# Optimization experiments

Measured on AMD Instinct MI355X. Metric: run time of the kernel, lower is better.

The kernel has to match this reference:

```python
import jax, jax.numpy as jnp
import numpy as np
from jax import lax

K_NEI = 64      # max_num_neighbors in radius query
NEG = -1e30     # mask value for max-aggregation


def fps(pos, n_sample):
    """Farthest point sampling per cloud. pos: [B,N,3] -> idx [B,n_sample] int32.
    Deterministic start at point 0 (PyG uses a random start)."""
    B, N, _ = pos.shape
    start = jnp.zeros((B,), jnp.int32)
    big = jnp.full((B, N), jnp.finfo(pos.dtype).max, pos.dtype)
    def body(carry, _):
        mind, last = carry
        lp = jnp.take_along_axis(pos, last[:, None, None], axis=1)  # [B,1,3]
        d = jnp.sum((pos - lp) ** 2, -1)                            # [B,N]
        mind = jnp.minimum(mind, d)
        nxt = jnp.argmax(mind, axis=1).astype(jnp.int32)
        return (mind, nxt), nxt
    (_, _), rest = lax.scan(body, (big, start), None, length=n_sample - 1)
    return jnp.concatenate([start[None], rest], 0).T  # [B, n_sample]


def radius_nn(pos_all, pos_q, r, k):
    """Up to k nearest neighbors within radius r (per cloud).
    pos_all: [B,N,3], pos_q: [B,M,3] -> idx [B,M,k] int32, valid [B,M,k] bool."""
    d2 = jnp.sum((pos_q[:, :, None, :] - pos_all[:, None, :, :]) ** 2, -1)  # [B,M,N]
    score = jnp.where(d2 <= r * r, -d2, -jnp.inf)
    vals, idx = lax.top_k(score, k)
    return idx, jnp.isfinite(vals)


def gather(feat, idx):
    """feat: [B,P,C], idx: [B,M,k] -> [B,M,k,C]"""
    B, M, k = idx.shape
    out = jnp.take_along_axis(feat, idx.reshape(B, M * k)[:, :, None], axis=1)
    return out.reshape(B, M, k, feat.shape[-1])


def mlp3(x, w1, b1, w2, b2, w3, b3):
    x = jax.nn.relu(x @ w1 + b1)
    x = jax.nn.relu(x @ w2 + b2)
    return x @ w3 + b3


def point_conv(x, pos_src, pos_dst, nidx, valid, params):
    """PyG PointConv: message = local_nn([x_j, pos_j - pos_i]), max aggregation."""
    rel = gather(pos_src, nidx) - pos_dst[:, :, None, :]          # [B,M,k,3]
    msg = rel if x is None else jnp.concatenate([gather(x, nidx), rel], -1)
    h = mlp3(msg, *params)                                        # [B,M,k,C]
    h = jnp.where(valid[..., None], h, NEG)
    out = jnp.max(h, axis=2)
    return jnp.where(valid.any(2)[..., None], out, 0.0)


def setup_inputs() -> dict:
    key = jax.random.key(0)
    shapes = {
        'sa1_w1': (3, 64), 'sa1_b1': (64,), 'sa1_w2': (64, 64), 'sa1_b2': (64,),
        'sa1_w3': (64, 128), 'sa1_b3': (128,),
        'sa2_w1': (131, 128), 'sa2_b1': (128,), 'sa2_w2': (128, 128), 'sa2_b2': (128,),
        'sa2_w3': (128, 256), 'sa2_b3': (256,),
        'g_w1': (259, 256), 'g_b1': (256,), 'g_w2': (256, 512), 'g_b2': (512,),
        'g_w3': (512, 1024), 'g_b3': (1024,),
        'l1_w': (1024, 512), 'l1_b': (512,), 'l2_w': (512, 256), 'l2_b': (256,),
        'l3_w': (256, 7), 'l3_b': (7,),
    }
    ks = jax.random.split(key, len(shapes) + 1)
    inp = {'points': jax.random.uniform(ks[0], (8, 4096, 3), jnp.float32)}
    for i, (name, shp) in enumerate(shapes.items()):
        inp[name] = jax.random.normal(ks[i + 1], shp, jnp.float32) / np.sqrt(shp[0]).astype(np.float32)
    return inp


def reference(points, sa1_w1, sa1_b1, sa1_w2, sa1_b2, sa1_w3, sa1_b3,
              sa2_w1, sa2_b1, sa2_w2, sa2_b2, sa2_w3, sa2_b3,
              g_w1, g_b1, g_w2, g_b2, g_w3, g_b3,
              l1_w, l1_b, l2_w, l2_b, l3_w, l3_b):
    B, N, _ = points.shape
    pos = points[..., :3]
    # ---- stage 1: fps ratio 0.5, radius 0.1 ----
    N1 = N // 2
    idx1 = fps(pos, N1)
    pos1 = jnp.take_along_axis(pos, idx1[..., None], axis=1)      # [B,N1,3]
    nidx1, valid1 = radius_nn(pos, pos1, 0.1, K_NEI)
    x1 = jax.nn.relu(point_conv(None, pos, pos1, nidx1, valid1,
                                (sa1_w1, sa1_b1, sa1_w2, sa1_b2, sa1_w3, sa1_b3)))
    # ---- stage 2: fps ratio 0.25, radius 0.2 ----
    N2 = N1 // 4
    idx2 = fps(pos1, N2)
    pos2 = jnp.take_along_axis(pos1, idx2[..., None], axis=1)     # [B,N2,3]
    nidx2, valid2 = radius_nn(pos1, pos2, 0.2, K_NEI)
    x2 = jax.nn.relu(point_conv(x1, pos1, pos2, nidx2, valid2,
                                (sa2_w1, sa2_b1, sa2_w2, sa2_b2, sa2_w3, sa2_b3)))
    # ---- global MLP + grouped maxpool over 128 points ----
    g = mlp3(jnp.concatenate([x2, pos2], -1), g_w1, g_b1, g_w2, g_b2, g_w3, g_b3)  # [B,N2,1024]
    g = g.reshape(-1, 128, 1024).max(axis=1)                      # [B*N2/128, 1024]
    h = jax.nn.relu(g @ l1_w + l1_b)                              # dropout = identity (eval)
    h = jax.nn.relu(h @ l2_w + l2_b)
    h = h @ l3_w + l3_b                                           # [B*N2/128, 7]
    b_out = h.reshape(B, -1, 7).mean(axis=1)                      # [B,7]
    t = b_out[:, :3]
    q = b_out[:, 3:]
    q = q / jnp.maximum(jnp.linalg.norm(q, axis=-1, keepdims=True), 1e-12)
    return jnp.concatenate([t, q], axis=-1)
```

## Files before the change

### kernel.cpp

```cpp
#include <hip/hip_runtime.h>
#include <float.h>


typedef float f32x2 __attribute__((ext_vector_type(2)));

__device__ __forceinline__ float d2_rn(float ax, float ay, float az,
                                       float bx, float by, float bz) {
  float dx = __fsub_rn(ax, bx), dy = __fsub_rn(ay, by), dz = __fsub_rn(az, bz);
  return __fadd_rn(__fadd_rn(__fmul_rn(dx, dx), __fmul_rn(dy, dy)), __fmul_rn(dz, dz));
}

template<int CTRL>
__device__ __forceinline__ unsigned long long dppmax(unsigned long long a) {
  const unsigned int lo = (unsigned int)a, hi = (unsigned int)(a >> 32);
  const unsigned int slo =
      (unsigned int)__builtin_amdgcn_update_dpp(0, (int)lo, CTRL, 0xf, 0xf, true);
  const unsigned int shi =
      (unsigned int)__builtin_amdgcn_update_dpp(0, (int)hi, CTRL, 0xf, 0xf, true);
  const unsigned long long s = ((unsigned long long)shi << 32) | slo;
  return s > a ? s : a;
}

template<int N, int NS, int T>
__global__ __launch_bounds__(T) void fps_kernel(const float* __restrict__ pos,
                                                float* __restrict__ posq) {
  constexpr int P = N / T;
  constexpr int W = T / 64;
  __shared__ float4 s_xyz[N];
  __shared__ unsigned long long s_red[2][W];
  const int t = threadIdx.x, b = blockIdx.x;
  const float* pb = pos + (size_t)b * N * 3;
  for (int i = t; i < N; i += T)
    s_xyz[i] = make_float4(pb[i*3+0], pb[i*3+1], pb[i*3+2], 0.f);
  __syncthreads();
  float px[P], py[P], pz[P], mind[P];
  unsigned int kc[P];
#pragma unroll
  for (int j = 0; j < P; ++j) {
    const float4 c = s_xyz[j*T + t];
    px[j] = c.x; py[j] = c.y; pz[j] = c.z;
    mind[j] = FLT_MAX;
    kc[j] = (unsigned int)(N - 1 - (j*T + t));
  }
  float lx = s_xyz[0].x, ly = s_xyz[0].y, lz = s_xyz[0].z;
  float* outp = posq + (size_t)b * NS * 3;
  if (t == 0) { outp[0] = lx; outp[1] = ly; outp[2] = lz; }
  for (int it = 1; it < NS; ++it) {
    float bv = -1.0f; unsigned int bk = 0;
#pragma unroll
    for (int j = 0; j < P; ++j) {
      const float dx = __fsub_rn(px[j], lx);
      const float dy = __fsub_rn(py[j], ly);
      const float dz = __fsub_rn(pz[j], lz);
      const float d = __fadd_rn(__fadd_rn(__fmul_rn(dx, dx), __fmul_rn(dy, dy)),
                                __fmul_rn(dz, dz));
      const float m = fminf(mind[j], d);
      mind[j] = m;
      const bool gt = m > bv;
      bv = gt ? m : bv;
      bk = gt ? kc[j] : bk;
    }
    unsigned long long key =
        ((unsigned long long)__float_as_uint(bv) << 32) | bk;
    key = dppmax<0x111>(key);
    key = dppmax<0x112>(key);
    key = dppmax<0x114>(key);
    key = dppmax<0x118>(key);
    key = dppmax<0x142>(key);
    key = dppmax<0x143>(key);
    const unsigned int wlo = (unsigned int)__builtin_amdgcn_readlane((int)(unsigned int)key, 63);
    const unsigned int whi = (unsigned int)__builtin_amdgcn_readlane((int)(unsigned int)(key >> 32), 63);
    unsigned long long best = ((unsigned long long)whi << 32) | wlo;
    if constexpr (W > 1) {
      const int par = it & 1;
      if ((t & 63) == 63) s_red[par][t >> 6] = best;
      __syncthreads();
#pragma unroll
      for (int w = 0; w < W; ++w) {
        const unsigned long long o = s_red[par][w];
        best = o > best ? o : best;
      }
    }
    const int idx = (N - 1) - (int)(unsigned int)(best & 0xFFFFFFFFull);
    const float4 c = s_xyz[idx];
    lx = c.x; ly = c.y; lz = c.z;
    if (t == 0) {
      outp[(size_t)it*3 + 0] = lx; outp[(size_t)it*3 + 1] = ly; outp[(size_t)it*3 + 2] = lz;
    }
  }
}

template<int CAP>
__global__ __launch_bounds__(128) void radius_kernel(
    const float* __restrict__ pall, const float* __restrict__ pq,
    int N, int M, float r2,
    int* __restrict__ nidx, int* __restrict__ ncnt) {
  const int bm = blockIdx.x;
  const int b = bm / M;
  const int t = threadIdx.x;
  __shared__ float s_d2[CAP];
  __shared__ int   s_id[CAP];
  __shared__ int   s_cnt;
  if (t == 0) s_cnt = 0;
  __syncthreads();
  const float* pb = pall + (size_t)b * N * 3;
  const float qx = pq[(size_t)bm*3], qy = pq[(size_t)bm*3+1], qz = pq[(size_t)bm*3+2];
  for (int i = t; i < N; i += 128) {
    const float d2 = d2_rn(qx, qy, qz, pb[i*3], pb[i*3+1], pb[i*3+2]);
    if (d2 <= r2) {
      const int p = atomicAdd(&s_cnt, 1);
      if (p < CAP) { s_d2[p] = d2; s_id[p] = i; }
    }
  }
  __syncthreads();
  const int cnt = min(s_cnt, CAP);
  int* out = nidx + (size_t)bm * 64;
  if (cnt <= 64) {
    if (t < cnt) out[t] = s_id[t];
    if (t == 0) ncnt[bm] = cnt;
  } else {
    for (int c = t; c < cnt; c += 128) {
      const float dc = s_d2[c]; const int ic = s_id[c];
      int rank = 0;
      for (int jj = 0; jj < cnt; ++jj)
        rank += (s_d2[jj] < dc) || (s_d2[jj] == dc && s_id[jj] < ic);
      if (rank < 64) out[rank] = s_id[c];
    }
    if (t == 0) ncnt[bm] = 64;
  }
}

__global__ __launch_bounds__(128, 4) void conv1_kernel(
    const float* __restrict__ pos, const float* __restrict__ posq,
    const int* __restrict__ nidx, const int* __restrict__ ncnt,
    const float* __restrict__ w1, const float* __restrict__ b1,
    const float* __restrict__ w2, const float* __restrict__ b2,
    const float* __restrict__ w3, const float* __restrict__ b3,
    float* __restrict__ xout) {
  const int bm = blockIdx.x;
  const int b  = bm >> 11;
  const int t  = threadIdx.x;
  const int j  = t & 63;
  const int g  = __builtin_amdgcn_readfirstlane(t >> 6);
  __shared__ float s_x[64 * 64];
  __shared__ float s_rel[64 * 4];
  __shared__ float s_out[128];
  const int cnt = ncnt[bm];
  float* outp = xout + (size_t)bm * 128;
  if (cnt == 0) { outp[t] = 0.f; return; }
  if (t < 64) {
    const int n = (t < cnt) ? nidx[(size_t)bm*64 + t] : 0;
    const float* p = pos + ((size_t)(b << 12) + n) * 3;
    const float qx = posq[(size_t)bm*3+0], qy = posq[(size_t)bm*3+1], qz = posq[(size_t)bm*3+2];
    s_rel[t*4+0] = p[0] - qx; s_rel[t*4+1] = p[1] - qy; s_rel[t*4+2] = p[2] - qz;
  }
  __syncthreads();
  const int sw  = (j & 15) << 1;
  const int row = j * 64;
  const float rx = s_rel[j*4+0], ry = s_rel[j*4+1], rz = s_rel[j*4+2];
  f32x2 acc[16];
  {
    const f32x2* bv = (const f32x2*)(b1 + g*32);
#pragma unroll
    for (int c = 0; c < 16; ++c) acc[c] = bv[c];
  }
#pragma unroll
  for (int kk = 0; kk < 3; ++kk) {
    const float xk = (kk == 0) ? rx : ((kk == 1) ? ry : rz);
    const f32x2 xv = {xk, xk};
    const float4* wr = (const float4*)(w1 + kk*64 + g*32);
#pragma unroll
    for (int c4 = 0; c4 < 8; ++c4) {
      const float4 w = wr[c4];
      acc[c4*2+0] += xv * f32x2{w.x, w.y};
      acc[c4*2+1] += xv * f32x2{w.z, w.w};
    }
  }
#pragma unroll
  for (int c = 0; c < 16; ++c) {
    f32x2 v = acc[c];
    v.x = fmaxf(v.x, 0.f); v.y = fmaxf(v.y, 0.f);
    *(f32x2*)(&s_x[row + ((g*32 + 2*c) ^ sw)]) = v;
  }
  __syncthreads();
  {
    const f32x2* bv = (const f32x2*)(b2 + g*32);
#pragma unroll
    for (int c = 0; c < 16; ++c) acc[c] = bv[c];
  }
#pragma unroll 2
  for (int k = 0; k < 64; ++k) {
    const float hk = s_x[row + (k ^ sw)];
    const f32x2 hv = {hk, hk};
    const float4* wr = (const float4*)(w2 + k*64 + g*32);
#pragma unroll
    for (int c4 = 0; c4 < 8; ++c4) {
      const float4 w = wr[c4];
      acc[c4*2+0] += hv * f32x2{w.x, w.y};
      acc[c4*2+1] += hv * f32x2{w.z, w.w};
    }
  }
  __syncthreads();
#pragma unroll
  for (int c = 0; c < 16; ++c) {
    f32x2 v = acc[c];
    v.x = fmaxf(v.x, 0.f); v.y = fmaxf(v.y, 0.f);
    *(f32x2*)(&s_x[row + ((g*32 + 2*c) ^ sw)]) = v;
  }
  __syncthreads();
#pragma unroll 1
  for (int p = 0; p < 2; ++p) {
    f32x2 a[16];
    {
      const f32x2* bv = (const f32x2*)(b3 + g*64 + p*32);
#pragma unroll
      for (int c = 0; c < 16; ++c) a[c] = bv[c];
    }
#pragma unroll 2
    for (int k = 0; k < 64; ++k) {
      const float hk = s_x[row + (k ^ sw)];
      const f32x2 hv = {hk, hk};
      const float4* wr = (const float4*)(w3 + k*128 + g*64 + p*32);
#pragma unroll
      for (int c4 = 0; c4 < 8; ++c4) {
        const float4 w = wr[c4];
        a[c4*2+0] += hv * f32x2{w.x, w.y};
        a[c4*2+1] += hv * f32x2{w.z, w.w};
      }
    }
    if (j >= cnt) {
#pragma unroll
      for (int c = 0; c < 16; ++c) a[c] = f32x2{-1e30f, -1e30f};
    }
#pragma unroll
    for (int off = 32; off > 0; off >>= 1) {
#pragma unroll
      for (int c = 0; c < 16; ++c) {
        a[c].x = fmaxf(a[c].x, __shfl_xor(a[c].x, off, 64));
        a[c].y = fmaxf(a[c].y, __shfl_xor(a[c].y, off, 64));
      }
    }
    if (j == 0) {
#pragma unroll
      for (int c = 0; c < 16; ++c) *(f32x2*)(&s_out[g*64 + p*32 + 2*c]) = a[c];
    }
  }
  __syncthreads();
  outp[t] = fmaxf(s_out[t], 0.f);
}

__global__ __launch_bounds__(256, 4) void conv2_kernel(
    const float* __restrict__ x1, const float* __restrict__ pos1, const float* __restrict__ pos2,
    const int* __restrict__ nidx, const int* __restrict__ ncnt,
    const float* __restrict__ w1, const float* __restrict__ b1,
    const float* __restrict__ w2, const float* __restrict__ b2,
    const float* __restrict__ w3, const float* __restrict__ b3,
    float* __restrict__ xout) {
  const int bm = blockIdx.x;
  const int b  = bm >> 9;
  const int t  = threadIdx.x;
  const int j  = t & 63;
  const int g  = __builtin_amdgcn_readfirstlane(t >> 6);
  __shared__ float s_x[64 * 128];
  __shared__ float s_rel[64 * 4];
  __shared__ int   s_n[64];
  __shared__ float s_out[256];
  const int cnt = ncnt[bm];
  float* outp = xout + (size_t)bm * 256;
  if (cnt == 0) { outp[t] = 0.f; return; }
  if (t < 64) {
    const int n = (t < cnt) ? nidx[(size_t)bm*64 + t] : 0;
    s_n[t] = n;
    const float* p = pos1 + ((size_t)(b << 11) + n) * 3;
    const float qx = pos2[(size_t)bm*3+0], qy = pos2[(size_t)bm*3+1], qz = pos2[(size_t)bm*3+2];
    s_rel[t*4+0] = p[0] - qx; s_rel[t*4+1] = p[1] - qy; s_rel[t*4+2] = p[2] - qz;
  }
  __syncthreads();
  for (int i = t; i < 64*128; i += 256) {
    const int r = i >> 7, c = i & 127;
    s_x[r*128 + (c ^ ((r & 15) << 1))] = x1[((size_t)(b << 11) + s_n[r])*128 + c];
  }
  __syncthreads();
  const int sw  = (j & 15) << 1;
  const int row = j * 128;
  f32x2 acc[16];
  {
    const f32x2* bv = (const f32x2*)(b1 + g*32);
#pragma unroll
    for (int c = 0; c < 16; ++c) acc[c] = bv[c];
  }
#pragma unroll 2
  for (int k = 0; k < 128; ++k) {
    const float xk = s_x[row + (k ^ sw)];
    const f32x2 xv = {xk, xk};
    const float4* wr = (const float4*)(w1 + k*128 + g*32);
#pragma unroll
    for (int c4 = 0; c4 < 8; ++c4) {
      const float4 w = wr[c4];
      acc[c4*2+0] += xv * f32x2{w.x, w.y};
      acc[c4*2+1] += xv * f32x2{w.z, w.w};
    }
  }
#pragma unroll
  for (int kk = 0; kk < 3; ++kk) {
    const float xk = s_rel[j*4 + kk];
    const f32x2 xv = {xk, xk};
    const float4* wr = (const float4*)(w1 + (128 + kk)*128 + g*32);
#pragma unroll
    for (int c4 = 0; c4 < 8; ++c4) {
      const float4 w = wr[c4];
      acc[c4*2+0] += xv * f32x2{w.x, w.y};
      acc[c4*2+1] += xv * f32x2{w.z, w.w};
    }
  }
  __syncthreads();
#pragma unroll
  for (int c = 0; c < 16; ++c) {
    f32x2 v = acc[c];
    v.x = fmaxf(v.x, 0.f); v.y = fmaxf(v.y, 0.f);
    *(f32x2*)(&s_x[row + ((g*32 + 2*c) ^ sw)]) = v;
  }
  __syncthreads();
  {
    const f32x2* bv = (const f32x2*)(b2 + g*32);
#pragma unroll
    for (int c = 0; c < 16; ++c) acc[c] = bv[c];
  }
#pragma unroll 2
  for (int k = 0; k < 128; ++k) {
    const float hk = s_x[row + (k ^ sw)];
    const f32x2 hv = {hk, hk};
    const float4* wr = (const float4*)(w2 + k*128 + g*32);
#pragma unroll
    for (int c4 = 0; c4 < 8; ++c4) {
      const float4 w = wr[c4];
      acc[c4*2+0] += hv * f32x2{w.x, w.y};
      acc[c4*2+1] += hv * f32x2{w.z, w.w};
    }
  }
  __syncthreads();
#pragma unroll
  for (int c = 0; c < 16; ++c) {
    f32x2 v = acc[c];
    v.x = fmaxf(v.x, 0.f); v.y = fmaxf(v.y, 0.f);
    *(f32x2*)(&s_x[row + ((g*32 + 2*c) ^ sw)]) = v;
  }
  __syncthreads();
#pragma unroll 1
  for (int p = 0; p < 2; ++p) {
    f32x2 a[16];
    {
      const f32x2* bv = (const f32x2*)(b3 + g*64 + p*32);
#pragma unroll
      for (int c = 0; c < 16; ++c) a[c] = bv[c];
    }
#pragma unroll 2
    for (int k = 0; k < 128; ++k) {
      const float hk = s_x[row + (k ^ sw)];
      const f32x2 hv = {hk, hk};
      const float4* wr = (const float4*)(w3 + k*256 + g*64 + p*32);
#pragma unroll
      for (int c4 = 0; c4 < 8; ++c4) {
        const float4 w = wr[c4];
        a[c4*2+0] += hv * f32x2{w.x, w.y};
        a[c4*2+1] += hv * f32x2{w.z, w.w};
      }
    }
    if (j >= cnt) {
#pragma unroll
      for (int c = 0; c < 16; ++c) a[c] = f32x2{-1e30f, -1e30f};
    }
#pragma unroll
    for (int off = 32; off > 0; off >>= 1) {
#pragma unroll
      for (int c = 0; c < 16; ++c) {
        a[c].x = fmaxf(a[c].x, __shfl_xor(a[c].x, off, 64));
        a[c].y = fmaxf(a[c].y, __shfl_xor(a[c].y, off, 64));
      }
    }
    if (j == 0) {
#pragma unroll
      for (int c = 0; c < 16; ++c) *(f32x2*)(&s_out[g*64 + p*32 + 2*c]) = a[c];
    }
  }
  __syncthreads();
  outp[t] = fmaxf(s_out[t], 0.f);
}

__global__ __launch_bounds__(256) void gmlp_kernel(
    const float* __restrict__ x2, const float* __restrict__ pos2,
    const float* __restrict__ w1, const float* __restrict__ b1,
    const float* __restrict__ w2, const float* __restrict__ b2,
    const float* __restrict__ w3, const float* __restrict__ b3,
    float* __restrict__ gpart) {
  const int blk = blockIdx.x;
  const int t = threadIdx.x;
  __shared__ float sA[260 * 18];
  __shared__ float sB[512 * 18];
  const int p0 = blk * 16;
  for (int i = t; i < 16*256; i += 256) {
    const int p = i >> 8, k = i & 255;
    sA[k*18 + p] = x2[(size_t)(p0 + p)*256 + k];
  }
  if (t < 48) { const int p = t/3, c = t%3; sA[(256+c)*18 + p] = pos2[(size_t)(p0+p)*3 + c]; }
  __syncthreads();
  f32x2 h1[8];
  { const float bb = b1[t];
#pragma unroll
    for (int p8 = 0; p8 < 8; ++p8) h1[p8] = f32x2{bb, bb}; }
#pragma unroll 2
  for (int k = 0; k < 259; ++k) {
    const float w = w1[(size_t)k*256 + t];
    const f32x2 wv = {w, w};
    const f32x2* row = (const f32x2*)(&sA[k*18]);
#pragma unroll
    for (int p8 = 0; p8 < 8; ++p8) h1[p8] += row[p8] * wv;
  }
  __syncthreads();
#pragma unroll
  for (int p8 = 0; p8 < 8; ++p8) {
    f32x2 a = h1[p8];
    a.x = fmaxf(a.x, 0.f); a.y = fmaxf(a.y, 0.f);
    *(f32x2*)(&sA[t*18 + 2*p8]) = a;
  }
  __syncthreads();
  f32x2 h2a[8], h2b[8];
  { const float ba = b2[t], bb = b2[t + 256];
#pragma unroll
    for (int p8 = 0; p8 < 8; ++p8) { h2a[p8] = f32x2{ba, ba}; h2b[p8] = f32x2{bb, bb}; } }
#pragma unroll 2
  for (int k = 0; k < 256; ++k) {
    const float wa = w2[(size_t)k*512 + t];
    const float wb = w2[(size_t)k*512 + t + 256];
    const f32x2 wav = {wa, wa}, wbv = {wb, wb};
    const f32x2* row = (const f32x2*)(&sA[k*18]);
#pragma unroll
    for (int p8 = 0; p8 < 8; ++p8) { const f32x2 x = row[p8]; h2a[p8] += x*wav; h2b[p8] += x*wbv; }
  }
  __syncthreads();
#pragma unroll
  for (int p8 = 0; p8 < 8; ++p8) {
    f32x2 a = h2a[p8], c = h2b[p8];
    a.x = fmaxf(a.x, 0.f); a.y = fmaxf(a.y, 0.f);
    c.x = fmaxf(c.x, 0.f); c.y = fmaxf(c.y, 0.f);
    *(f32x2*)(&sB[t*18 + 2*p8]) = a;
    *(f32x2*)(&sB[(t+256)*18 + 2*p8]) = c;
  }
  __syncthreads();
  f32x2 a3[4][8];
#pragma unroll
  for (int c = 0; c < 4; ++c) {
    const float bb = b3[t + c*256];
#pragma unroll
    for (int p8 = 0; p8 < 8; ++p8) a3[c][p8] = f32x2{bb, bb};
  }
#pragma unroll 2
  for (int k = 0; k < 512; ++k) {
    const f32x2* row = (const f32x2*)(&sB[k*18]);
    f32x2 xk[8];
#pragma unroll
    for (int p8 = 0; p8 < 8; ++p8) xk[p8] = row[p8];
#pragma unroll
    for (int c = 0; c < 4; ++c) {
      const float w = w3[(size_t)k*1024 + t + c*256];
      const f32x2 wv = {w, w};
#pragma unroll
      for (int p8 = 0; p8 < 8; ++p8) a3[c][p8] += xk[p8] * wv;
    }
  }
#pragma unroll
  for (int c = 0; c < 4; ++c) {
    f32x2 m2 = a3[c][0];
#pragma unroll
    for (int p8 = 1; p8 < 8; ++p8) {
      m2.x = fmaxf(m2.x, a3[c][p8].x); m2.y = fmaxf(m2.y, a3[c][p8].y);
    }
    gpart[(size_t)blk*1024 + t + c*256] = fmaxf(m2.x, m2.y);
  }
}

__global__ __launch_bounds__(256) void gmax_kernel(const float* __restrict__ gpart,
                                                   float* __restrict__ gmaxb) {
  const int g = blockIdx.x >> 2, chunk = blockIdx.x & 3;
  const int ch = chunk*256 + threadIdx.x;
  float v = gpart[(size_t)(g*8)*1024 + ch];
#pragma unroll
  for (int r = 1; r < 8; ++r) v = fmaxf(v, gpart[(size_t)(g*8 + r)*1024 + ch]);
  gmaxb[(size_t)g*1024 + ch] = v;
}

__global__ __launch_bounds__(256) void head_kernel(
    const float* __restrict__ gin,
    const float* __restrict__ l1w, const float* __restrict__ l1b,
    const float* __restrict__ l2w, const float* __restrict__ l2b,
    const float* __restrict__ l3w, const float* __restrict__ l3b,
    float* __restrict__ h3) {
  const int r = blockIdx.x, t = threadIdx.x;
  __shared__ float sIn[1024];
  __shared__ float sH[512];
  __shared__ float sH2[256];
  for (int i = t; i < 1024; i += 256) sIn[i] = gin[(size_t)r*1024 + i];
  __syncthreads();
  float a0 = l1b[t], a1 = l1b[t + 256];
#pragma unroll 4
  for (int k = 0; k < 1024; ++k) {
    const float x = sIn[k];
    a0 += x * l1w[(size_t)k*512 + t];
    a1 += x * l1w[(size_t)k*512 + t + 256];
  }
  sH[t] = fmaxf(a0, 0.f); sH[t+256] = fmaxf(a1, 0.f);
  __syncthreads();
  float a = l2b[t];
#pragma unroll 4
  for (int k = 0; k < 512; ++k) a += sH[k] * l2w[(size_t)k*256 + t];
  sH2[t] = fmaxf(a, 0.f);
  __syncthreads();
  if (t < 7) {
    float acc = l3b[t];
#pragma unroll 4
    for (int k = 0; k < 256; ++k) acc += sH2[k] * l3w[(size_t)k*7 + t];
    h3[(size_t)r*7 + t] = acc;
  }
}

__global__ void final_kernel(const float* __restrict__ h3, float* __restrict__ out) {
  const int b = threadIdx.x;
  if (b >= 8) return;
  float v[7];
#pragma unroll
  for (int c = 0; c < 7; ++c) {
    const float s = ((h3[(b*4+0)*7+c] + h3[(b*4+1)*7+c]) + h3[(b*4+2)*7+c]) + h3[(b*4+3)*7+c];
    v[c] = s * 0.25f;
  }
  const float nrm = fmaxf(sqrtf(((v[3]*v[3] + v[4]*v[4]) + v[5]*v[5]) + v[6]*v[6]), 1e-12f);
  out[b*7+0] = v[0]; out[b*7+1] = v[1]; out[b*7+2] = v[2];
  out[b*7+3] = v[3]/nrm; out[b*7+4] = v[4]/nrm;
  out[b*7+5] = v[5]/nrm; out[b*7+6] = v[6]/nrm;
}

extern "C" void kernel_launch(void* const* d_in, const int* in_sizes, int n_in,
                              void* d_out, int out_size, void* d_ws, size_t ws_size,
                              hipStream_t stream) {
  const float* points = (const float*)d_in[0];
  const float* sa1_w1 = (const float*)d_in[1];
  const float* sa1_b1 = (const float*)d_in[2];
  const float* sa1_w2 = (const float*)d_in[3];
  const float* sa1_b2 = (const float*)d_in[4];
  const float* sa1_w3 = (const float*)d_in[5];
  const float* sa1_b3 = (const float*)d_in[6];
  const float* sa2_w1 = (const float*)d_in[7];
  const float* sa2_b1 = (const float*)d_in[8];
  const float* sa2_w2 = (const float*)d_in[9];
  const float* sa2_b2 = (const float*)d_in[10];
  const float* sa2_w3 = (const float*)d_in[11];
  const float* sa2_b3 = (const float*)d_in[12];
  const float* g_w1   = (const float*)d_in[13];
  const float* g_b1   = (const float*)d_in[14];
  const float* g_w2   = (const float*)d_in[15];
  const float* g_b2   = (const float*)d_in[16];
  const float* g_w3   = (const float*)d_in[17];
  const float* g_b3   = (const float*)d_in[18];
  const float* l1_w   = (const float*)d_in[19];
  const float* l1_b   = (const float*)d_in[20];
  const float* l2_w   = (const float*)d_in[21];
  const float* l2_b   = (const float*)d_in[22];
  const float* l3_w   = (const float*)d_in[23];
  const float* l3_b   = (const float*)d_in[24];

  float* ws = (float*)d_ws;
  size_t o = 0;
  float* pos1  = ws + o; o += (size_t)8*2048*3;
  float* pos2  = ws + o; o += (size_t)8*512*3;
  int*   nidx1 = (int*)(ws + o); o += (size_t)8*2048*64;
  int*   ncnt1 = (int*)(ws + o); o += (size_t)8*2048;
  int*   nidx2 = (int*)(ws + o); o += (size_t)8*512*64;
  int*   ncnt2 = (int*)(ws + o); o += (size_t)8*512;
  float* x1    = ws + o; o += (size_t)8*2048*128;
  float* x2    = ws + o; o += (size_t)8*512*256;
  float* gpart = ws + o; o += (size_t)256*1024;
  float* gmaxb = ws + o; o += (size_t)32*1024;
  float* h3    = ws + o; o += (size_t)32*7;

  const float R2_1 = (float)(0.1 * 0.1);
  const float R2_2 = (float)(0.2 * 0.2);

  fps_kernel<4096, 2048, 256><<<8, 256, 0, stream>>>(points, pos1);
  radius_kernel<1024><<<8*2048, 128, 0, stream>>>(points, pos1, 4096, 2048, R2_1, nidx1, ncnt1);
  conv1_kernel<<<8*2048, 128, 0, stream>>>(points, pos1, nidx1, ncnt1,
                                           sa1_w1, sa1_b1, sa1_w2, sa1_b2, sa1_w3, sa1_b3, x1);
  fps_kernel<2048, 512, 256><<<8, 256, 0, stream>>>(pos1, pos2);
  radius_kernel<1024><<<8*512, 128, 0, stream>>>(pos1, pos2, 2048, 512, R2_2, nidx2, ncnt2);
  conv2_kernel<<<8*512, 256, 0, stream>>>(x1, pos1, pos2, nidx2, ncnt2,
                                          sa2_w1, sa2_b1, sa2_w2, sa2_b2, sa2_w3, sa2_b3, x2);
  gmlp_kernel<<<256, 256, 0, stream>>>(x2, pos2, g_w1, g_b1, g_w2, g_b2, g_w3, g_b3, gpart);
  gmax_kernel<<<128, 256, 0, stream>>>(gpart, gmaxb);
  head_kernel<<<32, 256, 0, stream>>>(gmaxb, l1_w, l1_b, l2_w, l2_b, l3_w, l3_b, h3);
  final_kernel<<<1, 64, 0, stream>>>(h3, (float*)d_out);
}
```

Before: 2.721 ms.

## Retune FPS block size, defer FPS output writes, fuse gmax into head

The FPS kernel now runs with 512 threads, which means fewer points per thread and more waves. The cross-wave reduction takes the last-lane DPP value directly and does a tree max over the wave slots. FPS also records the chosen indices in shared memory and writes all sampled coordinates after the loop, instead of having thread 0 do a global store every iteration. Separately, the gmax kernel is folded into the head kernel's input load, which removes one launch. The serial FPS loop dominates, so the gain depends on whether more waves offset the larger per-iteration barrier and reduction cost.

```diff
diff --git a/kernel.cpp b/kernel.cpp
--- a/kernel.cpp
+++ b/kernel.cpp
@@ -28,10 +28,12 @@
   constexpr int W = T / 64;
   __shared__ float4 s_xyz[N];
   __shared__ unsigned long long s_red[2][W];
+  __shared__ int s_idx[NS];
   const int t = threadIdx.x, b = blockIdx.x;
   const float* pb = pos + (size_t)b * N * 3;
   for (int i = t; i < N; i += T)
     s_xyz[i] = make_float4(pb[i*3+0], pb[i*3+1], pb[i*3+2], 0.f);
+  if (t == 0) s_idx[0] = 0;
   __syncthreads();
   float px[P], py[P], pz[P], mind[P];
   unsigned int kc[P];
@@ -43,8 +45,6 @@
     kc[j] = (unsigned int)(N - 1 - (j*T + t));
   }
   float lx = s_xyz[0].x, ly = s_xyz[0].y, lz = s_xyz[0].z;
-  float* outp = posq + (size_t)b * NS * 3;
-  if (t == 0) { outp[0] = lx; outp[1] = ly; outp[2] = lz; }
   for (int it = 1; it < NS; ++it) {
     float bv = -1.0f; unsigned int bk = 0;
 #pragma unroll
@@ -68,25 +68,27 @@
     key = dppmax<0x118>(key);
     key = dppmax<0x142>(key);
     key = dppmax<0x143>(key);
-    const unsigned int wlo = (unsigned int)__builtin_amdgcn_readlane((int)(unsigned int)key, 63);
-    const unsigned int whi = (unsigned int)__builtin_amdgcn_readlane((int)(unsigned int)(key >> 32), 63);
-    unsigned long long best = ((unsigned long long)whi << 32) | wlo;
-    if constexpr (W > 1) {
-      const int par = it & 1;
-      if ((t & 63) == 63) s_red[par][t >> 6] = best;
-      __syncthreads();
-#pragma unroll
-      for (int w = 0; w < W; ++w) {
-        const unsigned long long o = s_red[par][w];
-        best = o > best ? o : best;
-      }
-    }
+    const int par = it & 1;
+    if ((t & 63) == 63) s_red[par][t >> 6] = key;
+    __syncthreads();
+    unsigned long long v[W];
+#pragma unroll
+    for (int w = 0; w < W; ++w) v[w] = s_red[par][w];
+#pragma unroll
+    for (int s2 = W/2; s2 > 0; s2 >>= 1)
+#pragma unroll
+      for (int w = 0; w < s2; ++w) v[w] = v[w] >= v[w+s2] ? v[w] : v[w+s2];
+    const unsigned long long best = v[0];
     const int idx = (N - 1) - (int)(unsigned int)(best & 0xFFFFFFFFull);
+    if (t == 0) s_idx[it] = idx;
     const float4 c = s_xyz[idx];
     lx = c.x; ly = c.y; lz = c.z;
-    if (t == 0) {
-      outp[(size_t)it*3 + 0] = lx; outp[(size_t)it*3 + 1] = ly; outp[(size_t)it*3 + 2] = lz;
-    }
+  }
+  __syncthreads();
+  float* outp = posq + (size_t)b * NS * 3;
+  for (int s = t; s < NS; s += T) {
+    const float4 c = s_xyz[s_idx[s]];
+    outp[(size_t)s*3 + 0] = c.x; outp[(size_t)s*3 + 1] = c.y; outp[(size_t)s*3 + 2] = c.z;
   }
 }
 
@@ -479,18 +481,8 @@
   }
 }
 
-__global__ __launch_bounds__(256) void gmax_kernel(const float* __restrict__ gpart,
-                                                   float* __restrict__ gmaxb) {
-  const int g = blockIdx.x >> 2, chunk = blockIdx.x & 3;
-  const int ch = chunk*256 + threadIdx.x;
-  float v = gpart[(size_t)(g*8)*1024 + ch];
-#pragma unroll
-  for (int r = 1; r < 8; ++r) v = fmaxf(v, gpart[(size_t)(g*8 + r)*1024 + ch]);
-  gmaxb[(size_t)g*1024 + ch] = v;
-}
-
 __global__ __launch_bounds__(256) void head_kernel(
-    const float* __restrict__ gin,
+    const float* __restrict__ gpart,
     const float* __restrict__ l1w, const float* __restrict__ l1b,
     const float* __restrict__ l2w, const float* __restrict__ l2b,
     const float* __restrict__ l3w, const float* __restrict__ l3b,
@@ -499,7 +491,12 @@
   __shared__ float sIn[1024];
   __shared__ float sH[512];
   __shared__ float sH2[256];
-  for (int i = t; i < 1024; i += 256) sIn[i] = gin[(size_t)r*1024 + i];
+  for (int i = t; i < 1024; i += 256) {
+    float v = gpart[(size_t)(r*8)*1024 + i];
+#pragma unroll
+    for (int rr = 1; rr < 8; ++rr) v = fmaxf(v, gpart[(size_t)(r*8 + rr)*1024 + i]);
+    sIn[i] = v;
+  }
   __syncthreads();
   float a0 = l1b[t], a1 = l1b[t + 256];
 #pragma unroll 4
@@ -580,20 +577,20 @@
   float* gpart = ws + o; o += (size_t)256*1024;
   float* gmaxb = ws + o; o += (size_t)32*1024;
   float* h3    = ws + o; o += (size_t)32*7;
+  (void)gmaxb;
 
   const float R2_1 = (float)(0.1 * 0.1);
   const float R2_2 = (float)(0.2 * 0.2);
 
-  fps_kernel<4096, 2048, 256><<<8, 256, 0, stream>>>(points, pos1);
+  fps_kernel<4096, 2048, 512><<<8, 512, 0, stream>>>(points, pos1);
   radius_kernel<1024><<<8*2048, 128, 0, stream>>>(points, pos1, 4096, 2048, R2_1, nidx1, ncnt1);
   conv1_kernel<<<8*2048, 128, 0, stream>>>(points, pos1, nidx1, ncnt1,
                                            sa1_w1, sa1_b1, sa1_w2, sa1_b2, sa1_w3, sa1_b3, x1);
-  fps_kernel<2048, 512, 256><<<8, 256, 0, stream>>>(pos1, pos2);
+  fps_kernel<2048, 512, 512><<<8, 512, 0, stream>>>(pos1, pos2);
   radius_kernel<1024><<<8*512, 128, 0, stream>>>(pos1, pos2, 2048, 512, R2_2, nidx2, ncnt2);
   conv2_kernel<<<8*512, 256, 0, stream>>>(x1, pos1, pos2, nidx2, ncnt2,
                                           sa2_w1, sa2_b1, sa2_w2, sa2_b2, sa2_w3, sa2_b3, x2);
   gmlp_kernel<<<256, 256, 0, stream>>>(x2, pos2, g_w1, g_b1, g_w2, g_b2, g_w3, g_b3, gpart);
-  gmax_kernel<<<128, 256, 0, stream>>>(gpart, gmaxb);
-  head_kernel<<<32, 256, 0, stream>>>(gmaxb, l1_w, l1_b, l2_w, l2_b, l3_w, l3_b, h3);
+  head_kernel<<<32, 256, 0, stream>>>(gpart, l1_w, l1_b, l2_w, l2_b, l3_w, l3_b, h3);
   final_kernel<<<1, 64, 0, stream>>>(h3, (float*)d_out);
 }
```

New measurement: 2.803 ms. 3.0% more time.
